# Performance work log

Measured on AMD Instinct MI355X. Metric: run time of the kernel, lower is better.

## Reference

```python
import jax, jax.numpy as jnp
import numpy as np

ITER_ROUTING = 3


def squash(t):
    # t: [..., H]
    norm = jnp.sum(t * t, axis=-1)                      # [...]
    scale = norm / (1.0 + norm)
    return scale[..., None] * t / jnp.sqrt(norm)[..., None]


def setup_inputs() -> dict:
    key = jax.random.key(0)
    k1, k2 = jax.random.split(key)
    C, K, H = 1024, 64, 512  # H = 2 * hidden_size, hidden_size = 256
    encoder_output = jax.random.normal(k1, (C, K, H), dtype=jnp.float32)
    # nn.Linear(H, H, bias=False): weight W has shape [H_out, H_in], y = x @ W.T
    W = jax.random.normal(k2, (H, H), dtype=jnp.float32) * (1.0 / np.sqrt(H))
    return {"encoder_output": encoder_output, "W": W}


def reference(encoder_output, W):
    C, K, H = encoder_output.shape
    # Linear projection is identical every iteration in the original loop;
    # compute once (same math, same values).
    x_hat = jnp.einsum('ckh,gh->ckg', encoder_output, W)  # [C, K, H]
    b = jnp.zeros((C, K), dtype=encoder_output.dtype)
    c = None
    for _ in range(ITER_ROUTING):
        d = jax.nn.softmax(b, axis=-1)                    # [C, K]
        c_hat = jnp.sum(x_hat * d[..., None], axis=1)     # [C, H]
        c = squash(c_hat)                                 # [C, H]
        b = b + jnp.einsum('ckh,ch->ck', x_hat, c)        # agreement update
    return c
```

## Files before the change

### kernel.cpp

```cpp
#include <hip/hip_runtime.h>
#include <math.h>


#define KC 64
#define HD 512
#define NT 512

typedef _Float16 half8  __attribute__((ext_vector_type(8)));
typedef _Float16 half4v __attribute__((ext_vector_type(4)));
typedef float    f32x4  __attribute__((ext_vector_type(4)));

__launch_bounds__(256)
__global__ void cast_w_kernel(const float* __restrict__ W, _Float16* __restrict__ Wp) {
    int u    = blockIdx.x * 256 + threadIdx.x;
    int lane = u & 63;
    int j    = (u >> 6) & 3;
    int ks   = (u >> 8) & 1;
    int hs   = (u >> 9) & 7;
    int wv   = (u >> 12) & 7;
    int g  = wv * 64 + j * 16 + (lane & 15);
    int h0 = hs * 64 + ks * 32 + (lane >> 4) * 8;
    const float4* src = reinterpret_cast<const float4*>(W + (size_t)g * HD + h0);
    float4 a = src[0], b = src[1];
    half8 h = { (_Float16)a.x, (_Float16)a.y, (_Float16)a.z, (_Float16)a.w,
                (_Float16)b.x, (_Float16)b.y, (_Float16)b.z, (_Float16)b.w };
    *reinterpret_cast<half8*>(Wp + (size_t)u * 8) = h;
}

__launch_bounds__(NT, 2)
__global__ void routing_kernel(const float* __restrict__ enc,
                               const _Float16* __restrict__ Wp,
                               float* __restrict__ out) {
    __shared__ _Float16 slab[2][8][64][8];
    __shared__ float chatL[HD];
    __shared__ float bvec[KC];
    __shared__ float dvec[KC];
    __shared__ float bpart[8][KC];
    __shared__ float red[8];
    __shared__ float s_alpha;

    const int tid  = threadIdx.x;
    const int lane = tid & 63;
    const int wave = tid >> 6;
    const int l15  = lane & 15, l4 = lane >> 4;
    const int c    = blockIdx.x;
    const float* ebase = enc + (size_t)c * (KC * HD);
    const _Float16* wbase = Wp + ((size_t)wave << 15) + (lane << 3);

    if (tid < KC) bvec[tid] = 0.0f;

    f32x4 acc[16];
    #pragma unroll
    for (int i = 0; i < 16; ++i) acc[i] = (f32x4){0.f, 0.f, 0.f, 0.f};

    const int r0   = tid >> 4;
    const int c40  = (tid & 15) << 2;
    const int ks_w = c40 >> 5;
    const int l4g  = (c40 >> 3) & 3;
    const int e0w  = c40 & 7;
    const int prow = (l4g * 16 + (r0 & 15)) ^ (l4g << 1);
    const int p0   = (r0 >> 4) * 2 + ks_w;
    const int p1   = p0 + 4;
    const int plane_r = lane ^ ((lane >> 4) << 1);

    float4 ev0, ev1;
    auto eload = [&](int hs) {
        ev0 = *reinterpret_cast<const float4*>(ebase + (size_t)r0 * HD + hs * 64 + c40);
        ev1 = *reinterpret_cast<const float4*>(ebase + (size_t)(r0 + 32) * HD + hs * 64 + c40);
    };
    auto ewrite = [&](int b) {
        half4v h0 = { (_Float16)ev0.x, (_Float16)ev0.y, (_Float16)ev0.z, (_Float16)ev0.w };
        half4v h1 = { (_Float16)ev1.x, (_Float16)ev1.y, (_Float16)ev1.z, (_Float16)ev1.w };
        *reinterpret_cast<half4v*>(&slab[b][p0][prow][e0w]) = h0;
        *reinterpret_cast<half4v*>(&slab[b][p1][prow][e0w]) = h1;
    };

    half8 bf[2][8];
    auto bload = [&](int hs) {
        #pragma unroll
        for (int q = 0; q < 8; ++q)
            bf[hs & 1][q] = *reinterpret_cast<const half8*>(wbase + hs * 4096 + q * 512);
    };

    bload(0);
    eload(0);
    ewrite(0);

    #pragma unroll
    for (int hs = 0; hs < 8; ++hs) {
        __syncthreads();
        if (hs < 7) { eload(hs + 1); bload(hs + 1); }
        #pragma unroll
        for (int ks = 0; ks < 2; ++ks) {
            half8 af[4];
            #pragma unroll
            for (int i = 0; i < 4; ++i)
                af[i] = *reinterpret_cast<const half8*>(&slab[hs & 1][i * 2 + ks][plane_r][0]);
            #pragma unroll
            for (int i = 0; i < 4; ++i)
                #pragma unroll
                for (int j = 0; j < 4; ++j)
                    acc[i * 4 + j] = __builtin_amdgcn_mfma_f32_16x16x32_f16(
                        af[i], bf[hs & 1][ks * 4 + j], acc[i * 4 + j], 0, 0, 0);
        }
        if (hs < 7) ewrite((hs + 1) & 1);
    }
    __syncthreads();

    for (int it = 0; it < 3; ++it) {
        if (it > 0) {
            if (wave == 0) {
                float v = bvec[lane];
                float m = v;
                #pragma unroll
                for (int off = 32; off; off >>= 1) m = fmaxf(m, __shfl_xor(m, off));
                float e = expf(v - m);
                float s = e;
                #pragma unroll
                for (int off = 32; off; off >>= 1) s += __shfl_xor(s, off);
                dvec[lane] = e / s;
            }
            __syncthreads();
        }

        float chv[4];
        #pragma unroll
        for (int j = 0; j < 4; ++j) chv[j] = 0.f;
        #pragma unroll
        for (int i = 0; i < 4; ++i)
            #pragma unroll
            for (int r = 0; r < 4; ++r) {
                float dk = (it == 0) ? (1.0f / 64.0f) : dvec[i * 16 + l4 * 4 + r];
                #pragma unroll
                for (int j = 0; j < 4; ++j)
                    chv[j] += dk * acc[i * 4 + j][r];
            }
        #pragma unroll
        for (int j = 0; j < 4; ++j) {
            chv[j] += __shfl_xor(chv[j], 16);
            chv[j] += __shfl_xor(chv[j], 32);
        }
        if (l4 == 0) {
            #pragma unroll
            for (int j = 0; j < 4; ++j)
                chatL[wave * 64 + j * 16 + l15] = chv[j];
        }
        {
            float p = chv[0] * chv[0] + chv[1] * chv[1] + chv[2] * chv[2] + chv[3] * chv[3];
            #pragma unroll
            for (int off = 1; off <= 8; off <<= 1) p += __shfl_xor(p, off);
            if (lane == 0) red[wave] = p;
        }
        __syncthreads();
        if (tid == 0) {
            float n2 = red[0] + red[1] + red[2] + red[3] + red[4] + red[5] + red[6] + red[7];
            s_alpha = sqrtf(n2) / (1.0f + n2);
        }
        __syncthreads();

        if (it < 2) {
            #pragma unroll
            for (int i = 0; i < 4; ++i)
                #pragma unroll
                for (int r = 0; r < 4; ++r) {
                    float s = acc[i * 4 + 0][r] * chv[0]
                            + acc[i * 4 + 1][r] * chv[1]
                            + acc[i * 4 + 2][r] * chv[2]
                            + acc[i * 4 + 3][r] * chv[3];
                    #pragma unroll
                    for (int off = 1; off <= 8; off <<= 1) s += __shfl_xor(s, off);
                    if (l15 == 0) bpart[wave][i * 16 + l4 * 4 + r] = s;
                }
            __syncthreads();
            if (tid < KC) {
                float t = 0.f;
                #pragma unroll
                for (int w = 0; w < 8; ++w) t += bpart[w][tid];
                bvec[tid] += s_alpha * t;
            }
            __syncthreads();
        } else {
            out[(size_t)c * HD + tid] = s_alpha * chatL[tid];
        }
    }
}

extern "C" void kernel_launch(void* const* d_in, const int* in_sizes, int n_in,
                              void* d_out, int out_size, void* d_ws, size_t ws_size,
                              hipStream_t stream) {
    const float* enc = (const float*)d_in[0];
    const float* W   = (const float*)d_in[1];
    float* out       = (float*)d_out;
    _Float16* Wp     = (_Float16*)d_ws;
    (void)in_sizes; (void)n_in; (void)ws_size; (void)out_size;

    cast_w_kernel<<<128, 256, 0, stream>>>(W, Wp);
    routing_kernel<<<1024, NT, 0, stream>>>(enc, Wp, out);
}
```

Measured before the change: 81.15 us.

## Process four capsules per block with cross-capsule double-buffered encoder prefetch

Each block now handles four capsules in sequence instead of one, and launches 256 blocks instead of 1024. While the MFMA projection and the routing iterations run for one capsule, the next capsule's full encoder slab is loaded, converted to fp16 and written into a second LDS buffer. The aim is to hide global-load latency behind compute and routing. In exchange, LDS grows to about 128KB, which likely cuts occupancy to one block per CU. The grid drops to 256 blocks, which may leave CUs idle on a device with that many units.

```diff
diff --git a/kernel.cpp b/kernel.cpp
--- a/kernel.cpp
+++ b/kernel.cpp
@@ -5,6 +5,7 @@
 #define KC 64
 #define HD 512
 #define NT 512
+#define CPB4 4
 
 typedef _Float16 half8  __attribute__((ext_vector_type(8)));
 typedef _Float16 half4v __attribute__((ext_vector_type(4)));
@@ -31,7 +32,7 @@
 __global__ void routing_kernel(const float* __restrict__ enc,
                                const _Float16* __restrict__ Wp,
                                float* __restrict__ out) {
-    __shared__ _Float16 slab[2][8][64][8];
+    __shared__ _Float16 slab[2][8][8][64][8];
     __shared__ float chatL[HD];
     __shared__ float bvec[KC];
     __shared__ float dvec[KC];
@@ -43,15 +44,8 @@
     const int lane = tid & 63;
     const int wave = tid >> 6;
     const int l15  = lane & 15, l4 = lane >> 4;
-    const int c    = blockIdx.x;
-    const float* ebase = enc + (size_t)c * (KC * HD);
+    const int cbase = blockIdx.x * CPB4;
     const _Float16* wbase = Wp + ((size_t)wave << 15) + (lane << 3);
-
-    if (tid < KC) bvec[tid] = 0.0f;
-
-    f32x4 acc[16];
-    #pragma unroll
-    for (int i = 0; i < 16; ++i) acc[i] = (f32x4){0.f, 0.f, 0.f, 0.f};
 
     const int r0   = tid >> 4;
     const int c40  = (tid & 15) << 2;
@@ -63,124 +57,146 @@
     const int p1   = p0 + 4;
     const int plane_r = lane ^ ((lane >> 4) << 1);
 
-    float4 ev0, ev1;
-    auto eload = [&](int hs) {
-        ev0 = *reinterpret_cast<const float4*>(ebase + (size_t)r0 * HD + hs * 64 + c40);
-        ev1 = *reinterpret_cast<const float4*>(ebase + (size_t)(r0 + 32) * HD + hs * 64 + c40);
+    float4 ev[2][2];
+    half8  bf[2][8];
+
+    auto eload = [&](int cap, int hs, int sel) {
+        const float* eb = enc + (size_t)(cbase + cap) * (KC * HD);
+        ev[sel][0] = *reinterpret_cast<const float4*>(eb + (size_t)r0 * HD + hs * 64 + c40);
+        ev[sel][1] = *reinterpret_cast<const float4*>(eb + (size_t)(r0 + 32) * HD + hs * 64 + c40);
     };
-    auto ewrite = [&](int b) {
-        half4v h0 = { (_Float16)ev0.x, (_Float16)ev0.y, (_Float16)ev0.z, (_Float16)ev0.w };
-        half4v h1 = { (_Float16)ev1.x, (_Float16)ev1.y, (_Float16)ev1.z, (_Float16)ev1.w };
-        *reinterpret_cast<half4v*>(&slab[b][p0][prow][e0w]) = h0;
-        *reinterpret_cast<half4v*>(&slab[b][p1][prow][e0w]) = h1;
+    auto ewrite = [&](int buf, int hs, int sel) {
+        float4 v0 = ev[sel][0], v1 = ev[sel][1];
+        half4v h0 = { (_Float16)v0.x, (_Float16)v0.y, (_Float16)v0.z, (_Float16)v0.w };
+        half4v h1 = { (_Float16)v1.x, (_Float16)v1.y, (_Float16)v1.z, (_Float16)v1.w };
+        *reinterpret_cast<half4v*>(&slab[buf][hs][p0][prow][e0w]) = h0;
+        *reinterpret_cast<half4v*>(&slab[buf][hs][p1][prow][e0w]) = h1;
     };
-
-    half8 bf[2][8];
-    auto bload = [&](int hs) {
+    auto bload = [&](int hs, int sel) {
         #pragma unroll
         for (int q = 0; q < 8; ++q)
-            bf[hs & 1][q] = *reinterpret_cast<const half8*>(wbase + hs * 4096 + q * 512);
+            bf[sel][q] = *reinterpret_cast<const half8*>(wbase + hs * 4096 + q * 512);
     };
 
-    bload(0);
-    eload(0);
-    ewrite(0);
-
+    eload(0, 0, 0);
+    eload(0, 1, 1);
     #pragma unroll
-    for (int hs = 0; hs < 8; ++hs) {
+    for (int q = 0; q < 8; ++q) {
+        ewrite(0, q, q & 1);
+        if (q + 2 < 8) eload(0, q + 2, q & 1);
+    }
+
+    f32x4 acc[16];
+
+    for (int cap = 0; cap < CPB4; ++cap) {
+        const int cur = cap & 1;
+        const int nxt = cur ^ 1;
+        const bool st = (cap < CPB4 - 1);
+
         __syncthreads();
-        if (hs < 7) { eload(hs + 1); bload(hs + 1); }
+
         #pragma unroll
-        for (int ks = 0; ks < 2; ++ks) {
-            half8 af[4];
+        for (int i = 0; i < 16; ++i) acc[i] = (f32x4){0.f, 0.f, 0.f, 0.f};
+        if (tid < KC) bvec[tid] = 0.0f;
+
+        if (st) eload(cap + 1, 0, 0);
+        bload(0, 0);
+
+        #pragma unroll
+        for (int hs = 0; hs < 8; ++hs) {
+            if (hs < 7) bload(hs + 1, (hs + 1) & 1);
+            if (st && hs < 7) eload(cap + 1, hs + 1, (hs + 1) & 1);
+            #pragma unroll
+            for (int ks = 0; ks < 2; ++ks) {
+                half8 af[4];
+                #pragma unroll
+                for (int i = 0; i < 4; ++i)
+                    af[i] = *reinterpret_cast<const half8*>(&slab[cur][hs][i * 2 + ks][plane_r][0]);
+                #pragma unroll
+                for (int i = 0; i < 4; ++i)
+                    #pragma unroll
+                    for (int j = 0; j < 4; ++j)
+                        acc[i * 4 + j] = __builtin_amdgcn_mfma_f32_16x16x32_f16(
+                            af[i], bf[hs & 1][ks * 4 + j], acc[i * 4 + j], 0, 0, 0);
+            }
+            if (st) ewrite(nxt, hs, hs & 1);
+        }
+
+        for (int it = 0; it < 3; ++it) {
+            if (it > 0) {
+                if (wave == 0) {
+                    float v = bvec[lane];
+                    float m = v;
+                    #pragma unroll
+                    for (int off = 32; off; off >>= 1) m = fmaxf(m, __shfl_xor(m, off));
+                    float e = expf(v - m);
+                    float s = e;
+                    #pragma unroll
+                    for (int off = 32; off; off >>= 1) s += __shfl_xor(s, off);
+                    dvec[lane] = e / s;
+                }
+                __syncthreads();
+            }
+
+            float chv[4];
+            #pragma unroll
+            for (int j = 0; j < 4; ++j) chv[j] = 0.f;
             #pragma unroll
             for (int i = 0; i < 4; ++i)
-                af[i] = *reinterpret_cast<const half8*>(&slab[hs & 1][i * 2 + ks][plane_r][0]);
-            #pragma unroll
-            for (int i = 0; i < 4; ++i)
+                #pragma unroll
+                for (int r = 0; r < 4; ++r) {
+                    float dk = (it == 0) ? (1.0f / 64.0f) : dvec[i * 16 + l4 * 4 + r];
+                    #pragma unroll
+                    for (int j = 0; j < 4; ++j)
+                        chv[j] += dk * acc[i * 4 + j][r];
+                }
+            #pragma unroll
+            for (int j = 0; j < 4; ++j) {
+                chv[j] += __shfl_xor(chv[j], 16);
+                chv[j] += __shfl_xor(chv[j], 32);
+            }
+            if (l4 == 0) {
                 #pragma unroll
                 for (int j = 0; j < 4; ++j)
-                    acc[i * 4 + j] = __builtin_amdgcn_mfma_f32_16x16x32_f16(
-                        af[i], bf[hs & 1][ks * 4 + j], acc[i * 4 + j], 0, 0, 0);
-        }
-        if (hs < 7) ewrite((hs + 1) & 1);
-    }
-    __syncthreads();
-
-    for (int it = 0; it < 3; ++it) {
-        if (it > 0) {
-            if (wave == 0) {
-                float v = bvec[lane];
-                float m = v;
-                #pragma unroll
-                for (int off = 32; off; off >>= 1) m = fmaxf(m, __shfl_xor(m, off));
-                float e = expf(v - m);
-                float s = e;
-                #pragma unroll
-                for (int off = 32; off; off >>= 1) s += __shfl_xor(s, off);
-                dvec[lane] = e / s;
+                    chatL[wave * 64 + j * 16 + l15] = chv[j];
+            }
+            {
+                float p = chv[0] * chv[0] + chv[1] * chv[1] + chv[2] * chv[2] + chv[3] * chv[3];
+                #pragma unroll
+                for (int off = 1; off <= 8; off <<= 1) p += __shfl_xor(p, off);
+                if (lane == 0) red[wave] = p;
             }
             __syncthreads();
-        }
-
-        float chv[4];
-        #pragma unroll
-        for (int j = 0; j < 4; ++j) chv[j] = 0.f;
-        #pragma unroll
-        for (int i = 0; i < 4; ++i)
-            #pragma unroll
-            for (int r = 0; r < 4; ++r) {
-                float dk = (it == 0) ? (1.0f / 64.0f) : dvec[i * 16 + l4 * 4 + r];
-                #pragma unroll
-                for (int j = 0; j < 4; ++j)
-                    chv[j] += dk * acc[i * 4 + j][r];
-            }
-        #pragma unroll
-        for (int j = 0; j < 4; ++j) {
-            chv[j] += __shfl_xor(chv[j], 16);
-            chv[j] += __shfl_xor(chv[j], 32);
-        }
-        if (l4 == 0) {
-            #pragma unroll
-            for (int j = 0; j < 4; ++j)
-                chatL[wave * 64 + j * 16 + l15] = chv[j];
-        }
-        {
-            float p = chv[0] * chv[0] + chv[1] * chv[1] + chv[2] * chv[2] + chv[3] * chv[3];
-            #pragma unroll
-            for (int off = 1; off <= 8; off <<= 1) p += __shfl_xor(p, off);
-            if (lane == 0) red[wave] = p;
-        }
-        __syncthreads();
-        if (tid == 0) {
-            float n2 = red[0] + red[1] + red[2] + red[3] + red[4] + red[5] + red[6] + red[7];
-            s_alpha = sqrtf(n2) / (1.0f + n2);
-        }
-        __syncthreads();
-
-        if (it < 2) {
-            #pragma unroll
-            for (int i = 0; i < 4; ++i)
-                #pragma unroll
-                for (int r = 0; r < 4; ++r) {
-                    float s = acc[i * 4 + 0][r] * chv[0]
-                            + acc[i * 4 + 1][r] * chv[1]
-                            + acc[i * 4 + 2][r] * chv[2]
-                            + acc[i * 4 + 3][r] * chv[3];
-                    #pragma unroll
-                    for (int off = 1; off <= 8; off <<= 1) s += __shfl_xor(s, off);
-                    if (l15 == 0) bpart[wave][i * 16 + l4 * 4 + r] = s;
+            if (tid == 0) {
+                float n2 = red[0] + red[1] + red[2] + red[3] + red[4] + red[5] + red[6] + red[7];
+                s_alpha = sqrtf(n2) / (1.0f + n2);
+            }
+            __syncthreads();
+
+            if (it < 2) {
+                #pragma unroll
+                for (int i = 0; i < 4; ++i)
+                    #pragma unroll
+                    for (int r = 0; r < 4; ++r) {
+                        float s = acc[i * 4 + 0][r] * chv[0]
+                                + acc[i * 4 + 1][r] * chv[1]
+                                + acc[i * 4 + 2][r] * chv[2]
+                                + acc[i * 4 + 3][r] * chv[3];
+                        #pragma unroll
+                        for (int off = 1; off <= 8; off <<= 1) s += __shfl_xor(s, off);
+                        if (l15 == 0) bpart[wave][i * 16 + l4 * 4 + r] = s;
+                    }
+                __syncthreads();
+                if (tid < KC) {
+                    float t = 0.f;
+                    #pragma unroll
+                    for (int w = 0; w < 8; ++w) t += bpart[w][tid];
+                    bvec[tid] += s_alpha * t;
                 }
-            __syncthreads();
-            if (tid < KC) {
-                float t = 0.f;
-                #pragma unroll
-                for (int w = 0; w < 8; ++w) t += bpart[w][tid];
-                bvec[tid] += s_alpha * t;
-            }
-            __syncthreads();
-        } else {
-            out[(size_t)c * HD + tid] = s_alpha * chatL[tid];
+                __syncthreads();
+            } else {
+                out[(size_t)(cbase + cap) * HD + tid] = s_alpha * chatL[tid];
+            }
         }
     }
 }
@@ -195,5 +211,5 @@
     (void)in_sizes; (void)n_in; (void)ws_size; (void)out_size;
 
     cast_w_kernel<<<128, 256, 0, stream>>>(W, Wp);
-    routing_kernel<<<1024, NT, 0, stream>>>(enc, Wp, out);
+    routing_kernel<<<256, NT, 0, stream>>>(enc, Wp, out);
 }
```

New measurement: 131.5 us. 1.62x slower.

## Deepen encoder prefetch and make routing iterations barrier-light with redundant per-wave softmax

Applied to the files above, without the earlier changes.

Encoder loads now run three chunks ahead in a ring of register slots, which is meant to hide more global-memory latency during the MFMA projection. The routing loop drops the single-thread alpha step and the single-wave softmax. Every wave now redundantly sums the partial norms and agreement dots, then computes the softmax itself, using double-buffered shared arrays, so each iteration needs one barrier instead of several. Launch bounds drop to one block per CU minimum, which frees registers for the deeper prefetch but may lower occupancy.

```diff
diff --git a/kernel.cpp b/kernel.cpp
--- a/kernel.cpp
+++ b/kernel.cpp
@@ -27,17 +27,14 @@
     *reinterpret_cast<half8*>(Wp + (size_t)u * 8) = h;
 }
 
-__launch_bounds__(NT, 2)
+__launch_bounds__(NT, 1)
 __global__ void routing_kernel(const float* __restrict__ enc,
                                const _Float16* __restrict__ Wp,
                                float* __restrict__ out) {
     __shared__ _Float16 slab[2][8][64][8];
     __shared__ float chatL[HD];
-    __shared__ float bvec[KC];
-    __shared__ float dvec[KC];
-    __shared__ float bpart[8][KC];
-    __shared__ float red[8];
-    __shared__ float s_alpha;
+    __shared__ float bpart[2][8][KC];
+    __shared__ float redp[2][8];
 
     const int tid  = threadIdx.x;
     const int lane = tid & 63;
@@ -46,12 +43,6 @@
     const int c    = blockIdx.x;
     const float* ebase = enc + (size_t)c * (KC * HD);
     const _Float16* wbase = Wp + ((size_t)wave << 15) + (lane << 3);
-
-    if (tid < KC) bvec[tid] = 0.0f;
-
-    f32x4 acc[16];
-    #pragma unroll
-    for (int i = 0; i < 16; ++i) acc[i] = (f32x4){0.f, 0.f, 0.f, 0.f};
 
     const int r0   = tid >> 4;
     const int c40  = (tid & 15) << 2;
@@ -63,33 +54,39 @@
     const int p1   = p0 + 4;
     const int plane_r = lane ^ ((lane >> 4) << 1);
 
-    float4 ev0, ev1;
-    auto eload = [&](int hs) {
-        ev0 = *reinterpret_cast<const float4*>(ebase + (size_t)r0 * HD + hs * 64 + c40);
-        ev1 = *reinterpret_cast<const float4*>(ebase + (size_t)(r0 + 32) * HD + hs * 64 + c40);
+    float4 ev[3][2];
+    half8  bf[2][8];
+
+    auto eload = [&](int hs, int slot) {
+        ev[slot][0] = *reinterpret_cast<const float4*>(ebase + (size_t)r0 * HD + hs * 64 + c40);
+        ev[slot][1] = *reinterpret_cast<const float4*>(ebase + (size_t)(r0 + 32) * HD + hs * 64 + c40);
     };
-    auto ewrite = [&](int b) {
-        half4v h0 = { (_Float16)ev0.x, (_Float16)ev0.y, (_Float16)ev0.z, (_Float16)ev0.w };
-        half4v h1 = { (_Float16)ev1.x, (_Float16)ev1.y, (_Float16)ev1.z, (_Float16)ev1.w };
-        *reinterpret_cast<half4v*>(&slab[b][p0][prow][e0w]) = h0;
-        *reinterpret_cast<half4v*>(&slab[b][p1][prow][e0w]) = h1;
+    auto ewrite = [&](int chunk, int slot) {
+        float4 v0 = ev[slot][0], v1 = ev[slot][1];
+        half4v h0 = { (_Float16)v0.x, (_Float16)v0.y, (_Float16)v0.z, (_Float16)v0.w };
+        half4v h1 = { (_Float16)v1.x, (_Float16)v1.y, (_Float16)v1.z, (_Float16)v1.w };
+        *reinterpret_cast<half4v*>(&slab[chunk & 1][p0][prow][e0w]) = h0;
+        *reinterpret_cast<half4v*>(&slab[chunk & 1][p1][prow][e0w]) = h1;
     };
-
-    half8 bf[2][8];
     auto bload = [&](int hs) {
         #pragma unroll
         for (int q = 0; q < 8; ++q)
             bf[hs & 1][q] = *reinterpret_cast<const half8*>(wbase + hs * 4096 + q * 512);
     };
 
+    f32x4 acc[16];
+    #pragma unroll
+    for (int i = 0; i < 16; ++i) acc[i] = (f32x4){0.f, 0.f, 0.f, 0.f};
+
+    eload(0, 0); eload(1, 1); eload(2, 2);
     bload(0);
-    eload(0);
-    ewrite(0);
+    ewrite(0, 0);
 
     #pragma unroll
     for (int hs = 0; hs < 8; ++hs) {
         __syncthreads();
-        if (hs < 7) { eload(hs + 1); bload(hs + 1); }
+        if (hs < 7) bload(hs + 1);
+        if (hs < 5) eload(hs + 3, hs % 3);
         #pragma unroll
         for (int ks = 0; ks < 2; ++ks) {
             half8 af[4];
@@ -103,84 +100,109 @@
                     acc[i * 4 + j] = __builtin_amdgcn_mfma_f32_16x16x32_f16(
                         af[i], bf[hs & 1][ks * 4 + j], acc[i * 4 + j], 0, 0, 0);
         }
-        if (hs < 7) ewrite((hs + 1) & 1);
+        if (hs < 7) ewrite(hs + 1, (hs + 1) % 3);
     }
-    __syncthreads();
-
-    for (int it = 0; it < 3; ++it) {
-        if (it > 0) {
-            if (wave == 0) {
-                float v = bvec[lane];
-                float m = v;
-                #pragma unroll
-                for (int off = 32; off; off >>= 1) m = fmaxf(m, __shfl_xor(m, off));
-                float e = expf(v - m);
-                float s = e;
-                #pragma unroll
-                for (int off = 32; off; off >>= 1) s += __shfl_xor(s, off);
-                dvec[lane] = e / s;
-            }
-            __syncthreads();
-        }
-
-        float chv[4];
+
+    float breg = 0.0f;
+    float chv[4];
+
+    {
         #pragma unroll
         for (int j = 0; j < 4; ++j) chv[j] = 0.f;
         #pragma unroll
         for (int i = 0; i < 4; ++i)
             #pragma unroll
             for (int r = 0; r < 4; ++r) {
-                float dk = (it == 0) ? (1.0f / 64.0f) : dvec[i * 16 + l4 * 4 + r];
-                #pragma unroll
-                for (int j = 0; j < 4; ++j)
-                    chv[j] += dk * acc[i * 4 + j][r];
+                #pragma unroll
+                for (int j = 0; j < 4; ++j)
+                    chv[j] += (1.0f / 64.0f) * acc[i * 4 + j][r];
             }
         #pragma unroll
         for (int j = 0; j < 4; ++j) {
             chv[j] += __shfl_xor(chv[j], 16);
             chv[j] += __shfl_xor(chv[j], 32);
         }
-        if (l4 == 0) {
-            #pragma unroll
-            for (int j = 0; j < 4; ++j)
-                chatL[wave * 64 + j * 16 + l15] = chv[j];
-        }
-        {
-            float p = chv[0] * chv[0] + chv[1] * chv[1] + chv[2] * chv[2] + chv[3] * chv[3];
-            #pragma unroll
-            for (int off = 1; off <= 8; off <<= 1) p += __shfl_xor(p, off);
-            if (lane == 0) red[wave] = p;
-        }
+        float p = chv[0] * chv[0] + chv[1] * chv[1] + chv[2] * chv[2] + chv[3] * chv[3];
+        #pragma unroll
+        for (int off = 1; off <= 8; off <<= 1) p += __shfl_xor(p, off);
+        if (lane == 0) redp[0][wave] = p;
+        #pragma unroll
+        for (int i = 0; i < 4; ++i)
+            #pragma unroll
+            for (int r = 0; r < 4; ++r) {
+                float s = acc[i * 4 + 0][r] * chv[0] + acc[i * 4 + 1][r] * chv[1]
+                        + acc[i * 4 + 2][r] * chv[2] + acc[i * 4 + 3][r] * chv[3];
+                #pragma unroll
+                for (int off = 1; off <= 8; off <<= 1) s += __shfl_xor(s, off);
+                if (l15 == 0) bpart[0][wave][i * 16 + l4 * 4 + r] = s;
+            }
         __syncthreads();
-        if (tid == 0) {
-            float n2 = red[0] + red[1] + red[2] + red[3] + red[4] + red[5] + red[6] + red[7];
-            s_alpha = sqrtf(n2) / (1.0f + n2);
-        }
-        __syncthreads();
+    }
+
+    #pragma unroll
+    for (int it = 1; it < 3; ++it) {
+        const int rp = (it - 1) & 1, wp = it & 1;
+        float n2 = 0.f;
+        #pragma unroll
+        for (int w = 0; w < 8; ++w) n2 += redp[rp][w];
+        float alpha = sqrtf(n2) / (1.0f + n2);
+        float dot = 0.f;
+        #pragma unroll
+        for (int w = 0; w < 8; ++w) dot += bpart[rp][w][lane];
+        breg += alpha * dot;
+        float m = breg;
+        #pragma unroll
+        for (int off = 32; off; off >>= 1) m = fmaxf(m, __shfl_xor(m, off));
+        float e = expf(breg - m);
+        float se = e;
+        #pragma unroll
+        for (int off = 32; off; off >>= 1) se += __shfl_xor(se, off);
+        float dl = e / se;
+        #pragma unroll
+        for (int j = 0; j < 4; ++j) chv[j] = 0.f;
+        #pragma unroll
+        for (int i = 0; i < 4; ++i)
+            #pragma unroll
+            for (int r = 0; r < 4; ++r) {
+                float dk = __shfl(dl, i * 16 + l4 * 4 + r);
+                #pragma unroll
+                for (int j = 0; j < 4; ++j)
+                    chv[j] += dk * acc[i * 4 + j][r];
+            }
+        #pragma unroll
+        for (int j = 0; j < 4; ++j) {
+            chv[j] += __shfl_xor(chv[j], 16);
+            chv[j] += __shfl_xor(chv[j], 32);
+        }
+        float p = chv[0] * chv[0] + chv[1] * chv[1] + chv[2] * chv[2] + chv[3] * chv[3];
+        #pragma unroll
+        for (int off = 1; off <= 8; off <<= 1) p += __shfl_xor(p, off);
+        if (lane == 0) redp[wp][wave] = p;
 
         if (it < 2) {
             #pragma unroll
             for (int i = 0; i < 4; ++i)
                 #pragma unroll
                 for (int r = 0; r < 4; ++r) {
-                    float s = acc[i * 4 + 0][r] * chv[0]
-                            + acc[i * 4 + 1][r] * chv[1]
-                            + acc[i * 4 + 2][r] * chv[2]
-                            + acc[i * 4 + 3][r] * chv[3];
+                    float s = acc[i * 4 + 0][r] * chv[0] + acc[i * 4 + 1][r] * chv[1]
+                            + acc[i * 4 + 2][r] * chv[2] + acc[i * 4 + 3][r] * chv[3];
                     #pragma unroll
                     for (int off = 1; off <= 8; off <<= 1) s += __shfl_xor(s, off);
-                    if (l15 == 0) bpart[wave][i * 16 + l4 * 4 + r] = s;
+                    if (l15 == 0) bpart[wp][wave][i * 16 + l4 * 4 + r] = s;
                 }
             __syncthreads();
-            if (tid < KC) {
-                float t = 0.f;
-                #pragma unroll
-                for (int w = 0; w < 8; ++w) t += bpart[w][tid];
-                bvec[tid] += s_alpha * t;
+        } else {
+            if (l4 == 0) {
+                #pragma unroll
+                for (int j = 0; j < 4; ++j)
+                    chatL[wave * 64 + j * 16 + l15] = chv[j];
             }
             __syncthreads();
-        } else {
-            out[(size_t)c * HD + tid] = s_alpha * chatL[tid];
+            float n2f = 0.f;
+            #pragma unroll
+            for (int w = 0; w < 8; ++w) n2f += redp[wp][w];
+            float alphaf = sqrtf(n2f) / (1.0f + n2f);
+            out[(size_t)c * HD + tid] = alphaf * chatL[tid];
         }
     }
 }
```

New measurement: 81.19 us. About the same (+0.1%).
